# Kernel optimization log

Measured on AMD Instinct MI355X. Metric: run time of the kernel, lower is better.

Reference implementation:

```python
import jax, jax.numpy as jnp
import numpy as np

EPS = 1e-10
TAU = 1.0


def setup_inputs() -> dict:
    key = jax.random.key(0)
    ks = jax.random.split(key, 5)
    n, d = 1024, 64
    h1, h2, out = 128, 64, 2
    X = jax.random.normal(ks[0], (n, d), dtype=jnp.float32)
    W1 = jax.random.normal(ks[1], (2 * d, h1), dtype=jnp.float32) * (1.0 / np.sqrt(2 * d))
    b1 = jnp.zeros((h1,), dtype=jnp.float32)
    W2 = jax.random.normal(ks[2], (h1, h2), dtype=jnp.float32) * (1.0 / np.sqrt(h1))
    b2 = jnp.zeros((h2,), dtype=jnp.float32)
    W3 = jax.random.normal(ks[3], (h2, out), dtype=jnp.float32) * (1.0 / np.sqrt(h2))
    b3 = jnp.zeros((out,), dtype=jnp.float32)
    u = jax.random.uniform(ks[4], (n, n, out), dtype=jnp.float32)
    return {"X": X, "W1": W1, "b1": b1, "W2": W2, "b2": b2, "W3": W3, "b3": b3, "u": u}


def _mlp(h, W1, b1, W2, b2, W3, b3):
    h = jax.nn.relu(h @ W1 + b1)
    h = jax.nn.relu(h @ W2 + b2)
    return h @ W3 + b3


def reference(X, W1, b1, W2, b2, W3, b3, u):
    n, d = X.shape
    # pairwise features: pair[i, j] = concat(x_i, x_j)  -> (n, n, 2d)
    pair = jnp.concatenate(
        [jnp.broadcast_to(X[:, None, :], (n, n, d)),
         jnp.broadcast_to(X[None, :, :], (n, n, d))], axis=-1)
    logits = _mlp(pair, W1, b1, W2, b2, W3, b3)  # (n, n, 2)
    # undirected: mlp(pair.permute(1,0,2))[i,j] == mlp(pair)[j,i] (row-wise MLP)
    logits = 0.5 * (logits + jnp.swapaxes(logits, 0, 1))
    # gumbel-softmax, hard=True (straight-through)
    g = -jnp.log(-jnp.log(u + EPS) + EPS)
    y_soft = jax.nn.softmax((logits + g) / TAU, axis=-1)
    y_hard = jax.nn.one_hot(jnp.argmax(y_soft, axis=-1), y_soft.shape[-1], dtype=y_soft.dtype)
    y = jax.lax.stop_gradient(y_hard - y_soft) + y_soft
    # narrow(dim=2, start=1, size=1).squeeze() -> adjacency (n, n)
    return y[..., 1]
```

## Files before the change

### kernel.cpp

```cpp
#include <hip/hip_runtime.h>
#include <hip/hip_bf16.h>

#define N 1024
#define D 64
#define H1 128
#define H2 64
#define FLAG_THRESH 0.015f
#define H1PAD 136

typedef _Float16 half8 __attribute__((ext_vector_type(8)));
typedef float float4v __attribute__((ext_vector_type(4)));

__global__ __launch_bounds__(128) void precompute_kernel(
    const float* __restrict__ X, const float* __restrict__ W1,
    const float* __restrict__ b1,
    double* __restrict__ A64, double* __restrict__ B64,
    _Float16* __restrict__ A16, _Float16* __restrict__ B16)
{
    int i = blockIdx.x;
    int k = threadIdx.x;
    double a = (double)b1[k];
    double b = 0.0;
    for (int c = 0; c < D; ++c) {
        double x = (double)X[i * D + c];
        a += x * (double)W1[c * H1 + k];
        b += x * (double)W1[(D + c) * H1 + k];
    }
    A64[i * H1 + k] = a;
    B64[i * H1 + k] = b;
    A16[i * H1 + k] = (_Float16)(float)a;
    B16[i * H1 + k] = (_Float16)(float)b;
}

__global__ __launch_bounds__(256, 3) void pair_mlp_kernel(
    const _Float16* __restrict__ A16, const _Float16* __restrict__ B16,
    const float* __restrict__ W2, const float* __restrict__ b2,
    const float* __restrict__ W3, float* __restrict__ dmat)
{
    __shared__ _Float16 As16[16 * H1PAD];
    __shared__ _Float16 Bs16[64 * H1PAD];
    __shared__ _Float16 W2t[64 * H1PAD];

    int tid = threadIdx.x;
    int it = blockIdx.x >> 4;
    int jt = blockIdx.x & 15;
    int ti = it << 4;
    int tj = jt << 6;

    {
        int row = tid >> 4;
        int col = (tid & 15) << 3;
        *(half8*)&As16[row * H1PAD + col] =
            *(const half8*)&A16[(size_t)(ti + row) * H1 + col];
    }
    #pragma unroll
    for (int r = 0; r < 4; ++r) {
        int v = tid + r * 256;
        int row = v >> 4;
        int col = (v & 15) << 3;
        *(half8*)&Bs16[row * H1PAD + col] =
            *(const half8*)&B16[(size_t)(tj + row) * H1 + col];
    }
    #pragma unroll
    for (int r = 0; r < 32; ++r) {
        int idx = tid + r * 256;
        int k = idx >> 6;
        int n = idx & 63;
        W2t[n * H1PAD + k] = (_Float16)W2[idx];
    }
    __syncthreads();

    int lane = tid & 63;
    int wave = tid >> 6;
    int quad = lane >> 4;
    int m = lane & 15;

    half8 afrag[4][4];
    #pragma unroll
    for (int ks = 0; ks < 4; ++ks)
        #pragma unroll
        for (int nt = 0; nt < 4; ++nt)
            afrag[ks][nt] = *(const half8*)&W2t[(m + 16 * nt) * H1PAD + quad * 8 + 32 * ks];

    float b2x[4][4], w3x[4][4];
    #pragma unroll
    for (int nt = 0; nt < 4; ++nt)
        #pragma unroll
        for (int reg = 0; reg < 4; ++reg) {
            int o = (quad << 2) + reg + (nt << 4);
            b2x[nt][reg] = b2[o];
            w3x[nt][reg] = W3[o * 2 + 1] - W3[o * 2 + 0];
        }

    const half8 zero8 = {0, 0, 0, 0, 0, 0, 0, 0};

    #pragma unroll 1
    for (int jq = 0; jq < 4; ++jq) {
        int jj0 = jq << 4;
        half8 hb[4];
        #pragma unroll
        for (int ks = 0; ks < 4; ++ks)
            hb[ks] = *(const half8*)&Bs16[(jj0 + m) * H1PAD + quad * 8 + 32 * ks];

        #pragma unroll 1
        for (int i4 = 0; i4 < 4; ++i4) {
            int ii = (wave << 2) + i4;

            float4v acc[4];
            #pragma unroll
            for (int nt = 0; nt < 4; ++nt)
                acc[nt] = (float4v){b2x[nt][0], b2x[nt][1], b2x[nt][2], b2x[nt][3]};

            #pragma unroll
            for (int ks = 0; ks < 4; ++ks) {
                half8 ha = *(const half8*)&As16[ii * H1PAD + quad * 8 + 32 * ks];
                half8 h = __builtin_elementwise_max(ha + hb[ks], zero8);
                #pragma unroll
                for (int nt = 0; nt < 4; ++nt)
                    acc[nt] = __builtin_amdgcn_mfma_f32_16x16x32_f16(afrag[ks][nt], h, acc[nt], 0, 0, 0);
            }

            float s = 0.f;
            #pragma unroll
            for (int nt = 0; nt < 4; ++nt)
                #pragma unroll
                for (int reg = 0; reg < 4; ++reg)
                    s = fmaf(fmaxf(acc[nt][reg], 0.f), w3x[nt][reg], s);
            s += __shfl_xor(s, 16, 64);
            s += __shfl_xor(s, 32, 64);
            if (quad == 0) {
                dmat[(size_t)(ti + ii) * N + (tj + jj0 + m)] = s;
            }
        }
    }
}

__global__ __launch_bounds__(256) void epilogue_repair_kernel(
    const float* __restrict__ dmat, const double* __restrict__ A64,
    const double* __restrict__ B64, const float* __restrict__ W2,
    const float* __restrict__ b2, const float* __restrict__ W3,
    const float* __restrict__ b3, const float* __restrict__ u,
    float* __restrict__ out)
{
    __shared__ float T1[32][33];
    __shared__ float T2[32][33];
    __shared__ unsigned int lflags[1024];
    __shared__ unsigned int lcnt;
    __shared__ double h1s[4][2][H1];

    int bi = blockIdx.x >> 5;
    int bj = blockIdx.x & 31;
    int i0 = bi * 32, j0 = bj * 32;
    int tid = threadIdx.x;
    int r = tid >> 3;
    int c4 = (tid & 7) << 2;
    if (tid == 0) lcnt = 0;

    int a = tid >> 3;
    int b0 = (tid & 7) << 2;
    int ij0 = (i0 + a) * N + (j0 + b0);

    float4 u01 = *(const float4*)&u[((size_t)ij0) * 2];
    float4 u23 = *(const float4*)&u[((size_t)ij0) * 2 + 4];

    *(float4*)&T1[r][c4] = *(const float4*)&dmat[(size_t)(i0 + r) * N + j0 + c4];
    *(float4*)&T2[r][c4] = *(const float4*)&dmat[(size_t)(j0 + r) * N + i0 + c4];
    __syncthreads();

    float b3d = b3[1] - b3[0];
    float uu[8] = {u01.x, u01.y, u01.z, u01.w, u23.x, u23.y, u23.z, u23.w};

    float4 res;
    float* resp = &res.x;
    #pragma unroll
    for (int q = 0; q < 4; ++q) {
        int b = b0 + q;
        float l0 = -__logf(uu[2 * q] + 1e-10f) + 1e-10f;
        float l1 = -__logf(uu[2 * q + 1] + 1e-10f) + 1e-10f;
        float Dv = 0.5f * (T1[a][b] + T2[b][a]) + b3d + __logf(l0 / l1);
        resp[q] = Dv > 0.f ? 1.f : 0.f;
        if (fabsf(Dv) < FLAG_THRESH) {
            unsigned int idx = atomicAdd(&lcnt, 1u);
            lflags[idx] = (unsigned int)(ij0 + q);
        }
    }
    *(float4*)&out[ij0] = res;

    __syncthreads();

    unsigned int nl = lcnt;
    int lane = tid & 63;
    int wave = tid >> 6;
    double w3dd = (double)W3[lane * 2 + 1] - (double)W3[lane * 2 + 0];
    double b2d = (double)b2[lane];

    for (unsigned int f = wave; f < nl; f += 4) {
        int ij = (int)lflags[f];
        int i = ij >> 10, j = ij & (N - 1);
        double uvd = 0.0;
        if (lane < 2) uvd = (double)u[(((size_t)ij) << 1) + lane];
        {
            int k0 = lane, k1 = lane + 64;
            double ai0 = A64[(size_t)i * H1 + k0], ai1 = A64[(size_t)i * H1 + k1];
            double aj0 = A64[(size_t)j * H1 + k0], aj1 = A64[(size_t)j * H1 + k1];
            double bi0 = B64[(size_t)i * H1 + k0], bi1 = B64[(size_t)i * H1 + k1];
            double bj0 = B64[(size_t)j * H1 + k0], bj1 = B64[(size_t)j * H1 + k1];
            double v;
            v = ai0 + bj0; h1s[wave][0][k0] = v > 0.0 ? v : 0.0;
            v = ai1 + bj1; h1s[wave][0][k1] = v > 0.0 ? v : 0.0;
            v = aj0 + bi0; h1s[wave][1][k0] = v > 0.0 ? v : 0.0;
            v = aj1 + bi1; h1s[wave][1][k1] = v > 0.0 ? v : 0.0;
        }
        asm volatile("s_waitcnt lgkmcnt(0)" ::: "memory");
        __builtin_amdgcn_wave_barrier();

        const double* __restrict__ hap = h1s[wave][0];
        const double* __restrict__ hbp = h1s[wave][1];
        double sa0 = 0.0, sa1 = 0.0, sa2 = 0.0, sa3 = 0.0;
        double sb0 = 0.0, sb1 = 0.0, sb2 = 0.0, sb3 = 0.0;
        #pragma unroll 2
        for (int k = 0; k < H1; k += 4) {
            double w0 = (double)W2[(k + 0) * H2 + lane];
            double w1 = (double)W2[(k + 1) * H2 + lane];
            double w2v = (double)W2[(k + 2) * H2 + lane];
            double w3v = (double)W2[(k + 3) * H2 + lane];
            sa0 += hap[k + 0] * w0;  sa1 += hap[k + 1] * w1;
            sa2 += hap[k + 2] * w2v; sa3 += hap[k + 3] * w3v;
            sb0 += hbp[k + 0] * w0;  sb1 += hbp[k + 1] * w1;
            sb2 += hbp[k + 2] * w2v; sb3 += hbp[k + 3] * w3v;
        }
        double sa = ((sa0 + sa1) + (sa2 + sa3)) + b2d;
        double sb = ((sb0 + sb1) + (sb2 + sb3)) + b2d;
        if (sa < 0.0) sa = 0.0;
        if (sb < 0.0) sb = 0.0;
        double da = sa * w3dd;
        double db = sb * w3dd;
        #pragma unroll
        for (int off = 32; off > 0; off >>= 1) {
            da += __shfl_down(da, off, 64);
            db += __shfl_down(db, off, 64);
        }
        double g = 0.0;
        if (lane < 2) g = -log(-log(uvd + 1e-10) + 1e-10);
        double g0 = __shfl(g, 0, 64);
        double g1 = __shfl(g, 1, 64);
        if (lane == 0) {
            double b3dd = (double)b3[1] - (double)b3[0];
            double Dv = 0.5 * (da + db) + b3dd + (g1 - g0);
            out[ij] = Dv > 0.0 ? 1.f : 0.f;
        }
        __builtin_amdgcn_wave_barrier();
    }
}

extern "C" void kernel_launch(void* const* d_in, const int* in_sizes, int n_in,
                              void* d_out, int out_size, void* d_ws, size_t ws_size,
                              hipStream_t stream) {
    const float* X  = (const float*)d_in[0];
    const float* W1 = (const float*)d_in[1];
    const float* b1 = (const float*)d_in[2];
    const float* W2 = (const float*)d_in[3];
    const float* b2 = (const float*)d_in[4];
    const float* W3 = (const float*)d_in[5];
    const float* b3 = (const float*)d_in[6];
    const float* u  = (const float*)d_in[7];
    float* out = (float*)d_out;

    double* A64 = (double*)d_ws;
    double* B64 = A64 + (size_t)N * H1;
    float* dmat = (float*)(B64 + (size_t)N * H1);
    _Float16* A16 = (_Float16*)(dmat + (size_t)N * N);
    _Float16* B16 = A16 + (size_t)N * H1;

    precompute_kernel<<<N, 128, 0, stream>>>(X, W1, b1, A64, B64, A16, B16);
    pair_mlp_kernel<<<(N / 16) * (N / 64), 256, 0, stream>>>(A16, B16, W2, b2, W3, dmat);
    epilogue_repair_kernel<<<(N / 32) * (N / 32), 256, 0, stream>>>(
        dmat, A64, B64, W2, b2, W3, b3, u, out);
}
```

Before: 131.2 us.

## Fuse pair MLP and epilogue over symmetric tile pairs, dropping dmat

Merges the pair MLP kernel and the epilogue/repair kernel into one kernel that processes upper-triangular 32x32 tile pairs, computing both the ij and ji directions in shared memory. This removes the global dmat write and read and one kernel launch. Shared memory is overlaid between the score tiles and the repair buffers, and a flag cap is added. It lowers occupancy (launch bounds 2) and uses 528 blocks, which may load-balance unevenly across CUs.

```diff
diff --git a/kernel.cpp b/kernel.cpp
--- a/kernel.cpp
+++ b/kernel.cpp
@@ -6,6 +6,7 @@
 #define H1 128
 #define H2 64
 #define FLAG_THRESH 0.015f
+#define FLAG_CAP 1024
 #define H1PAD 136
 
 typedef _Float16 half8 __attribute__((ext_vector_type(8)));
@@ -32,40 +33,43 @@
     B16[i * H1 + k] = (_Float16)(float)b;
 }
 
-__global__ __launch_bounds__(256, 3) void pair_mlp_kernel(
+__global__ __launch_bounds__(256, 2) void fused_pair_kernel(
     const _Float16* __restrict__ A16, const _Float16* __restrict__ B16,
+    const double* __restrict__ A64, const double* __restrict__ B64,
     const float* __restrict__ W2, const float* __restrict__ b2,
-    const float* __restrict__ W3, float* __restrict__ dmat)
+    const float* __restrict__ W3, const float* __restrict__ b3,
+    const float* __restrict__ u, float* __restrict__ out)
 {
-    __shared__ _Float16 As16[16 * H1PAD];
-    __shared__ _Float16 Bs16[64 * H1PAD];
+    __shared__ _Float16 Ar[64 * H1PAD];
+    __shared__ _Float16 Br[64 * H1PAD];
     __shared__ _Float16 W2t[64 * H1PAD];
+    __shared__ __align__(16) unsigned char overlay[2 * 32 * 33 * 4];
+    __shared__ unsigned int lflags[FLAG_CAP];
+    __shared__ unsigned int lcnt;
+
+    float (*Sij)[33] = (float(*)[33])overlay;
+    float (*Sji)[33] = (float(*)[33])(overlay + 32 * 33 * 4);
 
     int tid = threadIdx.x;
-    int it = blockIdx.x >> 4;
-    int jt = blockIdx.x & 15;
-    int ti = it << 4;
-    int tj = jt << 6;
-
-    {
-        int row = tid >> 4;
-        int col = (tid & 15) << 3;
-        *(half8*)&As16[row * H1PAD + col] =
-            *(const half8*)&A16[(size_t)(ti + row) * H1 + col];
-    }
-    #pragma unroll
-    for (int r = 0; r < 4; ++r) {
-        int v = tid + r * 256;
+    int t = blockIdx.x, ti = 0;
+    while (t >= 32 - ti) { t -= 32 - ti; ++ti; }
+    int tj = ti + t;
+    int I0 = ti << 5, J0 = tj << 5;
+    if (tid == 0) lcnt = 0;
+
+    #pragma unroll
+    for (int it = 0; it < 4; ++it) {
+        int v = tid + it * 256;
         int row = v >> 4;
         int col = (v & 15) << 3;
-        *(half8*)&Bs16[row * H1PAD + col] =
-            *(const half8*)&B16[(size_t)(tj + row) * H1 + col];
+        int gr = (row < 32) ? (I0 + row) : (J0 + row - 32);
+        *(half8*)&Ar[row * H1PAD + col] = *(const half8*)&A16[(size_t)gr * H1 + col];
+        *(half8*)&Br[row * H1PAD + col] = *(const half8*)&B16[(size_t)gr * H1 + col];
     }
     #pragma unroll
     for (int r = 0; r < 32; ++r) {
         int idx = tid + r * 256;
-        int k = idx >> 6;
-        int n = idx & 63;
+        int k = idx >> 6, n = idx & 63;
         W2t[n * H1PAD + k] = (_Float16)W2[idx];
     }
     __syncthreads();
@@ -94,103 +98,93 @@
 
     const half8 zero8 = {0, 0, 0, 0, 0, 0, 0, 0};
 
+    int dir = wave >> 1;
+    int jh = wave & 1;
+    int abase = dir ? 32 : 0;
+    int bbase = dir ? 0 : 32;
+    float (*Sout)[33] = dir ? Sji : Sij;
+
+    half8 hb[4];
+    #pragma unroll
+    for (int ks = 0; ks < 4; ++ks)
+        hb[ks] = *(const half8*)&Br[(bbase + jh * 16 + m) * H1PAD + quad * 8 + 32 * ks];
+
     #pragma unroll 1
-    for (int jq = 0; jq < 4; ++jq) {
-        int jj0 = jq << 4;
-        half8 hb[4];
-        #pragma unroll
-        for (int ks = 0; ks < 4; ++ks)
-            hb[ks] = *(const half8*)&Bs16[(jj0 + m) * H1PAD + quad * 8 + 32 * ks];
-
-        #pragma unroll 1
-        for (int i4 = 0; i4 < 4; ++i4) {
-            int ii = (wave << 2) + i4;
-
-            float4v acc[4];
+    for (int ii = 0; ii < 32; ++ii) {
+        float4v acc[4];
+        #pragma unroll
+        for (int nt = 0; nt < 4; ++nt)
+            acc[nt] = (float4v){b2x[nt][0], b2x[nt][1], b2x[nt][2], b2x[nt][3]};
+
+        #pragma unroll
+        for (int ks = 0; ks < 4; ++ks) {
+            half8 ha = *(const half8*)&Ar[(abase + ii) * H1PAD + quad * 8 + 32 * ks];
+            half8 h = __builtin_elementwise_max(ha + hb[ks], zero8);
             #pragma unroll
             for (int nt = 0; nt < 4; ++nt)
-                acc[nt] = (float4v){b2x[nt][0], b2x[nt][1], b2x[nt][2], b2x[nt][3]};
-
+                acc[nt] = __builtin_amdgcn_mfma_f32_16x16x32_f16(afrag[ks][nt], h, acc[nt], 0, 0, 0);
+        }
+        float s = 0.f;
+        #pragma unroll
+        for (int nt = 0; nt < 4; ++nt)
             #pragma unroll
-            for (int ks = 0; ks < 4; ++ks) {
-                half8 ha = *(const half8*)&As16[ii * H1PAD + quad * 8 + 32 * ks];
-                half8 h = __builtin_elementwise_max(ha + hb[ks], zero8);
-                #pragma unroll
-                for (int nt = 0; nt < 4; ++nt)
-                    acc[nt] = __builtin_amdgcn_mfma_f32_16x16x32_f16(afrag[ks][nt], h, acc[nt], 0, 0, 0);
+            for (int reg = 0; reg < 4; ++reg)
+                s = fmaf(fmaxf(acc[nt][reg], 0.f), w3x[nt][reg], s);
+        s += __shfl_xor(s, 16, 64);
+        s += __shfl_xor(s, 32, 64);
+        if (quad == 0) Sout[ii][jh * 16 + m] = s;
+    }
+    __syncthreads();
+
+    float b3d = b3[1] - b3[0];
+    {
+        int i = tid >> 3, j0 = (tid & 7) << 2;
+        int ij0 = (I0 + i) * N + (J0 + j0);
+        float4 u01 = *(const float4*)&u[((size_t)ij0) * 2];
+        float4 u23 = *(const float4*)&u[((size_t)ij0) * 2 + 4];
+        float uu[8] = {u01.x, u01.y, u01.z, u01.w, u23.x, u23.y, u23.z, u23.w};
+        float4 res; float* resp = &res.x;
+        #pragma unroll
+        for (int q = 0; q < 4; ++q) {
+            int j = j0 + q;
+            float l0 = -__logf(uu[2 * q] + 1e-10f) + 1e-10f;
+            float l1 = -__logf(uu[2 * q + 1] + 1e-10f) + 1e-10f;
+            float Dv = 0.5f * (Sij[i][j] + Sji[j][i]) + b3d + __logf(l0 / l1);
+            resp[q] = Dv > 0.f ? 1.f : 0.f;
+            if (fabsf(Dv) < FLAG_THRESH) {
+                unsigned int idx = atomicAdd(&lcnt, 1u);
+                if (idx < FLAG_CAP) lflags[idx] = (unsigned int)(ij0 + q);
             }
-
-            float s = 0.f;
-            #pragma unroll
-            for (int nt = 0; nt < 4; ++nt)
-                #pragma unroll
-                for (int reg = 0; reg < 4; ++reg)
-                    s = fmaf(fmaxf(acc[nt][reg], 0.f), w3x[nt][reg], s);
-            s += __shfl_xor(s, 16, 64);
-            s += __shfl_xor(s, 32, 64);
-            if (quad == 0) {
-                dmat[(size_t)(ti + ii) * N + (tj + jj0 + m)] = s;
+        }
+        *(float4*)&out[ij0] = res;
+    }
+    if (ti != tj) {
+        int j = tid >> 3, i0 = (tid & 7) << 2;
+        int ij0 = (J0 + j) * N + (I0 + i0);
+        float4 u01 = *(const float4*)&u[((size_t)ij0) * 2];
+        float4 u23 = *(const float4*)&u[((size_t)ij0) * 2 + 4];
+        float uu[8] = {u01.x, u01.y, u01.z, u01.w, u23.x, u23.y, u23.z, u23.w};
+        float4 res; float* resp = &res.x;
+        #pragma unroll
+        for (int q = 0; q < 4; ++q) {
+            int i = i0 + q;
+            float l0 = -__logf(uu[2 * q] + 1e-10f) + 1e-10f;
+            float l1 = -__logf(uu[2 * q + 1] + 1e-10f) + 1e-10f;
+            float Dv = 0.5f * (Sji[j][i] + Sij[i][j]) + b3d + __logf(l0 / l1);
+            resp[q] = Dv > 0.f ? 1.f : 0.f;
+            if (fabsf(Dv) < FLAG_THRESH) {
+                unsigned int idx = atomicAdd(&lcnt, 1u);
+                if (idx < FLAG_CAP) lflags[idx] = (unsigned int)(ij0 + q);
             }
         }
-    }
-}
-
-__global__ __launch_bounds__(256) void epilogue_repair_kernel(
-    const float* __restrict__ dmat, const double* __restrict__ A64,
-    const double* __restrict__ B64, const float* __restrict__ W2,
-    const float* __restrict__ b2, const float* __restrict__ W3,
-    const float* __restrict__ b3, const float* __restrict__ u,
-    float* __restrict__ out)
-{
-    __shared__ float T1[32][33];
-    __shared__ float T2[32][33];
-    __shared__ unsigned int lflags[1024];
-    __shared__ unsigned int lcnt;
-    __shared__ double h1s[4][2][H1];
-
-    int bi = blockIdx.x >> 5;
-    int bj = blockIdx.x & 31;
-    int i0 = bi * 32, j0 = bj * 32;
-    int tid = threadIdx.x;
-    int r = tid >> 3;
-    int c4 = (tid & 7) << 2;
-    if (tid == 0) lcnt = 0;
-
-    int a = tid >> 3;
-    int b0 = (tid & 7) << 2;
-    int ij0 = (i0 + a) * N + (j0 + b0);
-
-    float4 u01 = *(const float4*)&u[((size_t)ij0) * 2];
-    float4 u23 = *(const float4*)&u[((size_t)ij0) * 2 + 4];
-
-    *(float4*)&T1[r][c4] = *(const float4*)&dmat[(size_t)(i0 + r) * N + j0 + c4];
-    *(float4*)&T2[r][c4] = *(const float4*)&dmat[(size_t)(j0 + r) * N + i0 + c4];
+        *(float4*)&out[ij0] = res;
+    }
+
     __syncthreads();
 
-    float b3d = b3[1] - b3[0];
-    float uu[8] = {u01.x, u01.y, u01.z, u01.w, u23.x, u23.y, u23.z, u23.w};
-
-    float4 res;
-    float* resp = &res.x;
-    #pragma unroll
-    for (int q = 0; q < 4; ++q) {
-        int b = b0 + q;
-        float l0 = -__logf(uu[2 * q] + 1e-10f) + 1e-10f;
-        float l1 = -__logf(uu[2 * q + 1] + 1e-10f) + 1e-10f;
-        float Dv = 0.5f * (T1[a][b] + T2[b][a]) + b3d + __logf(l0 / l1);
-        resp[q] = Dv > 0.f ? 1.f : 0.f;
-        if (fabsf(Dv) < FLAG_THRESH) {
-            unsigned int idx = atomicAdd(&lcnt, 1u);
-            lflags[idx] = (unsigned int)(ij0 + q);
-        }
-    }
-    *(float4*)&out[ij0] = res;
-
-    __syncthreads();
-
     unsigned int nl = lcnt;
-    int lane = tid & 63;
-    int wave = tid >> 6;
+    if (nl > FLAG_CAP) nl = FLAG_CAP;
+    double (*h1s)[2][H1] = (double(*)[2][H1])overlay;
     double w3dd = (double)W3[lane * 2 + 1] - (double)W3[lane * 2 + 0];
     double b2d = (double)b2[lane];
 
@@ -268,12 +262,10 @@
 
     double* A64 = (double*)d_ws;
     double* B64 = A64 + (size_t)N * H1;
-    float* dmat = (float*)(B64 + (size_t)N * H1);
-    _Float16* A16 = (_Float16*)(dmat + (size_t)N * N);
+    _Float16* A16 = (_Float16*)(B64 + (size_t)N * H1);
     _Float16* B16 = A16 + (size_t)N * H1;
 
     precompute_kernel<<<N, 128, 0, stream>>>(X, W1, b1, A64, B64, A16, B16);
-    pair_mlp_kernel<<<(N / 16) * (N / 64), 256, 0, stream>>>(A16, B16, W2, b2, W3, dmat);
-    epilogue_repair_kernel<<<(N / 32) * (N / 32), 256, 0, stream>>>(
-        dmat, A64, B64, W2, b2, W3, b3, u, out);
+    fused_pair_kernel<<<528, 256, 0, stream>>>(A16, B16, A64, B64,
+                                               W2, b2, W3, b3, u, out);
 }
```

Result: slower. 151.8 us (+15.7%).

## Load W2 fragments directly from global, raise occupancy, retile epilogue to 16x64

Applied to the files above, without the earlier changes.

The pair MLP kernel no longer stages a transposed copy of W2 in shared memory. Each lane gathers its W2 fragments straight from global memory, which frees LDS so the launch bound can allow four blocks per CU. The epilogue tile changes from 32x32 to 16x64 to match the MLP tiling. The flag list is shrunk and capped at 256 entries, which reduces LDS use. Flags beyond the cap are silently dropped, so borderline entries could skip the FP64 repair. The strided scalar global gathers of W2 may also cost more than the old staged load.

```diff
diff --git a/kernel.cpp b/kernel.cpp
--- a/kernel.cpp
+++ b/kernel.cpp
@@ -6,6 +6,7 @@
 #define H1 128
 #define H2 64
 #define FLAG_THRESH 0.015f
+#define FLAG_CAP 256
 #define H1PAD 136
 
 typedef _Float16 half8 __attribute__((ext_vector_type(8)));
@@ -32,14 +33,13 @@
     B16[i * H1 + k] = (_Float16)(float)b;
 }
 
-__global__ __launch_bounds__(256, 3) void pair_mlp_kernel(
+__global__ __launch_bounds__(256, 4) void pair_mlp_kernel(
     const _Float16* __restrict__ A16, const _Float16* __restrict__ B16,
     const float* __restrict__ W2, const float* __restrict__ b2,
     const float* __restrict__ W3, float* __restrict__ dmat)
 {
     __shared__ _Float16 As16[16 * H1PAD];
     __shared__ _Float16 Bs16[64 * H1PAD];
-    __shared__ _Float16 W2t[64 * H1PAD];
 
     int tid = threadIdx.x;
     int it = blockIdx.x >> 4;
@@ -61,14 +61,6 @@
         *(half8*)&Bs16[row * H1PAD + col] =
             *(const half8*)&B16[(size_t)(tj + row) * H1 + col];
     }
-    #pragma unroll
-    for (int r = 0; r < 32; ++r) {
-        int idx = tid + r * 256;
-        int k = idx >> 6;
-        int n = idx & 63;
-        W2t[n * H1PAD + k] = (_Float16)W2[idx];
-    }
-    __syncthreads();
 
     int lane = tid & 63;
     int wave = tid >> 6;
@@ -79,8 +71,15 @@
     #pragma unroll
     for (int ks = 0; ks < 4; ++ks)
         #pragma unroll
-        for (int nt = 0; nt < 4; ++nt)
-            afrag[ks][nt] = *(const half8*)&W2t[(m + 16 * nt) * H1PAD + quad * 8 + 32 * ks];
+        for (int nt = 0; nt < 4; ++nt) {
+            int o = m + (nt << 4);
+            int kb = (quad << 3) + (ks << 5);
+            half8 f;
+            #pragma unroll
+            for (int j = 0; j < 8; ++j)
+                f[j] = (_Float16)W2[(kb + j) * H2 + o];
+            afrag[ks][nt] = f;
+        }
 
     float b2x[4][4], w3x[4][4];
     #pragma unroll
@@ -91,6 +90,8 @@
             b2x[nt][reg] = b2[o];
             w3x[nt][reg] = W3[o * 2 + 1] - W3[o * 2 + 0];
         }
+
+    __syncthreads();
 
     const half8 zero8 = {0, 0, 0, 0, 0, 0, 0, 0};
 
@@ -142,29 +143,33 @@
     const float* __restrict__ b3, const float* __restrict__ u,
     float* __restrict__ out)
 {
-    __shared__ float T1[32][33];
-    __shared__ float T2[32][33];
-    __shared__ unsigned int lflags[1024];
+    __shared__ float T1[16][65];
+    __shared__ float T2[64][19];
+    __shared__ unsigned int lflags[FLAG_CAP];
     __shared__ unsigned int lcnt;
     __shared__ double h1s[4][2][H1];
 
-    int bi = blockIdx.x >> 5;
-    int bj = blockIdx.x & 31;
-    int i0 = bi * 32, j0 = bj * 32;
+    int bi = blockIdx.x >> 4;
+    int bj = blockIdx.x & 15;
+    int i0 = bi << 4, j0 = bj << 6;
     int tid = threadIdx.x;
-    int r = tid >> 3;
-    int c4 = (tid & 7) << 2;
     if (tid == 0) lcnt = 0;
 
-    int a = tid >> 3;
-    int b0 = (tid & 7) << 2;
-    int ij0 = (i0 + a) * N + (j0 + b0);
+    int i = tid >> 4;
+    int jl0 = (tid & 15) << 2;
+    int ij0 = (i0 + i) * N + (j0 + jl0);
 
     float4 u01 = *(const float4*)&u[((size_t)ij0) * 2];
     float4 u23 = *(const float4*)&u[((size_t)ij0) * 2 + 4];
 
-    *(float4*)&T1[r][c4] = *(const float4*)&dmat[(size_t)(i0 + r) * N + j0 + c4];
-    *(float4*)&T2[r][c4] = *(const float4*)&dmat[(size_t)(j0 + r) * N + i0 + c4];
+    {
+        int row = tid >> 4, col = (tid & 15) << 2;
+        *(float4*)&T1[row][col] = *(const float4*)&dmat[(size_t)(i0 + row) * N + j0 + col];
+    }
+    {
+        int row = tid >> 2, col = (tid & 3) << 2;
+        *(float4*)&T2[row][col] = *(const float4*)&dmat[(size_t)(j0 + row) * N + i0 + col];
+    }
     __syncthreads();
 
     float b3d = b3[1] - b3[0];
@@ -174,14 +179,14 @@
     float* resp = &res.x;
     #pragma unroll
     for (int q = 0; q < 4; ++q) {
-        int b = b0 + q;
+        int j = jl0 + q;
         float l0 = -__logf(uu[2 * q] + 1e-10f) + 1e-10f;
         float l1 = -__logf(uu[2 * q + 1] + 1e-10f) + 1e-10f;
-        float Dv = 0.5f * (T1[a][b] + T2[b][a]) + b3d + __logf(l0 / l1);
+        float Dv = 0.5f * (T1[i][j] + T2[j][i]) + b3d + __logf(l0 / l1);
         resp[q] = Dv > 0.f ? 1.f : 0.f;
         if (fabsf(Dv) < FLAG_THRESH) {
             unsigned int idx = atomicAdd(&lcnt, 1u);
-            lflags[idx] = (unsigned int)(ij0 + q);
+            if (idx < FLAG_CAP) lflags[idx] = (unsigned int)(ij0 + q);
         }
     }
     *(float4*)&out[ij0] = res;
@@ -189,6 +194,7 @@
     __syncthreads();
 
     unsigned int nl = lcnt;
+    if (nl > FLAG_CAP) nl = FLAG_CAP;
     int lane = tid & 63;
     int wave = tid >> 6;
     double w3dd = (double)W3[lane * 2 + 1] - (double)W3[lane * 2 + 0];
@@ -196,15 +202,15 @@
 
     for (unsigned int f = wave; f < nl; f += 4) {
         int ij = (int)lflags[f];
-        int i = ij >> 10, j = ij & (N - 1);
+        int ii = ij >> 10, jj = ij & (N - 1);
         double uvd = 0.0;
         if (lane < 2) uvd = (double)u[(((size_t)ij) << 1) + lane];
         {
             int k0 = lane, k1 = lane + 64;
-            double ai0 = A64[(size_t)i * H1 + k0], ai1 = A64[(size_t)i * H1 + k1];
-            double aj0 = A64[(size_t)j * H1 + k0], aj1 = A64[(size_t)j * H1 + k1];
-            double bi0 = B64[(size_t)i * H1 + k0], bi1 = B64[(size_t)i * H1 + k1];
-            double bj0 = B64[(size_t)j * H1 + k0], bj1 = B64[(size_t)j * H1 + k1];
+            double ai0 = A64[(size_t)ii * H1 + k0], ai1 = A64[(size_t)ii * H1 + k1];
+            double aj0 = A64[(size_t)jj * H1 + k0], aj1 = A64[(size_t)jj * H1 + k1];
+            double bi0 = B64[(size_t)ii * H1 + k0], bi1 = B64[(size_t)ii * H1 + k1];
+            double bj0 = B64[(size_t)jj * H1 + k0], bj1 = B64[(size_t)jj * H1 + k1];
             double v;
             v = ai0 + bj0; h1s[wave][0][k0] = v > 0.0 ? v : 0.0;
             v = ai1 + bj1; h1s[wave][0][k1] = v > 0.0 ? v : 0.0;
@@ -274,6 +280,6 @@
 
     precompute_kernel<<<N, 128, 0, stream>>>(X, W1, b1, A64, B64, A16, B16);
     pair_mlp_kernel<<<(N / 16) * (N / 64), 256, 0, stream>>>(A16, B16, W2, b2, W3, dmat);
-    epilogue_repair_kernel<<<(N / 32) * (N / 32), 256, 0, stream>>>(
+    epilogue_repair_kernel<<<(N / 16) * (N / 64), 256, 0, stream>>>(
         dmat, A64, B64, W2, b2, W3, b3, u, out);
 }
```

Result: slower. 153.6 us (+17.1%).
